# Optimization experiments

Measured on AMD Instinct MI355X. Metric: run time of the kernel, lower is better.

Reference implementation:

```python
import jax, jax.numpy as jnp
import numpy as np

B, L, D = 8, 512, 32      # batch, seq_len, hidden_size (input dim)
N = 64                     # features_nodes (attention neurons)
H = 64                     # interm_layer_size (LSTM hidden)


def setup_inputs() -> dict:
    key = jax.random.key(0)
    ks = jax.random.split(key, 12)
    s = lambda k, shape, fan: jax.random.normal(k, shape, jnp.float32) * (1.0 / np.sqrt(fan))
    return {
        "text": jax.random.normal(ks[0], (B, L, D), jnp.float32),
        # AttentionLSTM params
        "Wx_w": s(ks[1], (N, D), D),
        "Wx_b": jnp.zeros((N,), jnp.float32),
        "Wxhat_w": s(ks[2], (N, D), D),
        "Wxhat_b": jnp.zeros((N,), jnp.float32),
        "att_w": s(ks[3], (1, N), N),
        "att_b": jnp.zeros((1,), jnp.float32),
        # unidirectional LSTM params (PyTorch layout: gates i,f,g,o)
        "W_ih": s(ks[4], (4 * H, D), D),
        "W_hh": s(ks[5], (4 * H, H), H),
        "b_ih": jnp.zeros((4 * H,), jnp.float32),
        "b_hh": jnp.zeros((4 * H,), jnp.float32),
        # dense head
        "dense_w": s(ks[6], (2, H), H),
        "dense_b": jnp.zeros((2,), jnp.float32),
    }


def _forward(text, Wx_w, Wx_b, Wxhat_w, Wxhat_b, att_w, att_b,
             W_ih, W_hh, b_ih, b_hh, dense_w, dense_b):
    # --- AttentionLSTM ---
    Wx = text @ Wx_w.T + Wx_b          # [B,L,N]
    # Wthat[b,i,j,:] = text[b,j,:], so Linear(Wthat) == Wxhat broadcast over i
    Wxhat = text @ Wxhat_w.T + Wxhat_b  # [B,L,N]
    # tanh(Wxhat[b,j] + Wx[b,i]) -> [B,L,L,N]
    t = jnp.tanh(Wxhat[:, None, :, :] + Wx[:, :, None, :])
    A = jax.nn.sigmoid(jnp.einsum('bijn,n->bij', t, att_w[0]) + att_b[0])  # [B,L,L]
    Xatt = jnp.einsum('bij,bjd->bid', A, text)  # sum_j Wthat*A -> [B,L,D]

    # --- unidirectional LSTM (last hidden state only) ---
    h0 = jnp.zeros((text.shape[0], H), text.dtype)
    c0 = jnp.zeros((text.shape[0], H), text.dtype)

    def step(carry, x_t):
        h, c = carry
        gates = x_t @ W_ih.T + b_ih + h @ W_hh.T + b_hh  # [B,4H]
        i, f, g, o = jnp.split(gates, 4, axis=-1)
        c = jax.nn.sigmoid(f) * c + jax.nn.sigmoid(i) * jnp.tanh(g)
        h = jax.nn.sigmoid(o) * jnp.tanh(c)
        return (h, c), None

    (h_last, _), _ = jax.lax.scan(step, (h0, c0), jnp.swapaxes(Xatt, 0, 1))
    return h_last @ dense_w.T + dense_b  # [B,2]


def reference(text, Wx_w, Wx_b, Wxhat_w, Wxhat_b, att_w, att_b,
              W_ih, W_hh, b_ih, b_hh, dense_w, dense_b):
    return _forward(text, Wx_w, Wx_b, Wxhat_w, Wxhat_b, att_w, att_b,
                    W_ih, W_hh, b_ih, b_hh, dense_w, dense_b)
```

## Files before the change

### kernel.cpp

```cpp
#include <hip/hip_runtime.h>
#include <hip/hip_bf16.h>

#define Bb 8
#define Ll 512
#define Dd 32
#define Nn 64
#define Hh 64
#define G4 256

#define L2E  1.4426950408889634f
#define L2E2 2.8853900817779268f

typedef _Float16 h2_t __attribute__((ext_vector_type(2)));

__device__ __forceinline__ float fast_rcp(float x) { return __builtin_amdgcn_rcpf(x); }
__device__ __forceinline__ float fast_exp2(float x) { return __builtin_amdgcn_exp2f(x); }

__device__ __forceinline__ float sig2(float x) {
    return fast_rcp(1.f + fast_exp2(-L2E * x));
}
__device__ __forceinline__ float tanh2(float x) {
    return fmaf(2.f, fast_rcp(1.f + fast_exp2(-L2E2 * x)), -1.f);
}

__device__ __forceinline__ float fdot2(h2_t a, h2_t b, float c) {
#if __has_builtin(__builtin_amdgcn_fdot2)
    return __builtin_amdgcn_fdot2(a, b, c, false);
#else
    return c + (float)a[0] * (float)b[0] + (float)a[1] * (float)b[1];
#endif
}

template<int CTRL>
__device__ __forceinline__ float quad_dpp(float v) {
    return __int_as_float(__builtin_amdgcn_mov_dpp(__float_as_int(v), CTRL, 0xf, 0xf, true));
}
__device__ __forceinline__ float quad_sum(float v) {
    v += quad_dpp<0xB1>(v);
    v += quad_dpp<0x4E>(v);
    return v;
}

__global__ __launch_bounds__(256) void k_proj(
    const float* __restrict__ text,
    const float* __restrict__ Wx_w, const float* __restrict__ Wx_b,
    const float* __restrict__ Wxh_w, const float* __restrict__ Wxh_b,
    float* __restrict__ Ex, float* __restrict__ Eh) {
    int idx = blockIdx.x * 256 + threadIdx.x;
    int n = idx & 63;
    int bl = idx >> 6;
    const float4* tr = (const float4*)(text + bl * Dd);
    const float4* w1 = (const float4*)(Wx_w + n * Dd);
    const float4* w2 = (const float4*)(Wxh_w + n * Dd);
    float a0 = 0.f, a1 = 0.f;
#pragma unroll
    for (int q = 0; q < 8; ++q) {
        float4 t4 = tr[q]; float4 x4 = w1[q]; float4 y4 = w2[q];
        a0 += t4.x * x4.x + t4.y * x4.y + t4.z * x4.z + t4.w * x4.w;
        a1 += t4.x * y4.x + t4.y * y4.y + t4.z * y4.z + t4.w * y4.w;
    }
    Ex[idx] = fast_exp2(L2E2 * (a0 + Wx_b[n]));
    Eh[idx] = fast_exp2(L2E2 * (a1 + Wxh_b[n]));
}

__global__ __launch_bounds__(256) void k_attn(
    const float* __restrict__ text,
    const float* __restrict__ Ex, const float* __restrict__ Eh,
    const float* __restrict__ att_w, const float* __restrict__ att_b,
    const float* __restrict__ W_ih, const float* __restrict__ b_ih,
    const float* __restrict__ b_hh, float* __restrict__ Gx) {
    __shared__ float s_eh[64 * 65];
    __shared__ float s_text[32 * 65];
    __shared__ float2 s_fa[4 * 64];
    __shared__ float s_A[4 * 64];
    __shared__ __align__(16) float s_xatt[4][32];

    int tid = threadIdx.x;
    int bx = blockIdx.x;
    int b = bx >> 7;
    int i0 = (bx & 127) << 2;
    int w = tid >> 6, l = tid & 63;
    int i = i0 + w;

    s_fa[w * 64 + l] = make_float2(Ex[((b * Ll) + i) * Nn + l], att_w[l]);
    float ab = att_b[0];
    __syncthreads();

    float awsum = 0.f;
#pragma unroll
    for (int n = 0; n < 64; ++n) awsum += s_fa[w * 64 + n].y;
    float zc = awsum + ab;

    float xacc = 0.f;
    int d = l & 31, hf = l >> 5;

    for (int jt = 0; jt < 8; ++jt) {
        __syncthreads();
        {
            int n = tid & 63; int j4 = tid >> 6;
#pragma unroll
            for (int r = 0; r < 16; ++r) {
                int jl = j4 + r * 4;
                s_eh[n * 65 + jl] = Eh[((b * Ll) + jt * 64 + jl) * Nn + n];
            }
            int dd = tid & 31; int j8 = tid >> 5;
#pragma unroll
            for (int r = 0; r < 8; ++r) {
                int jl = j8 + r * 8;
                s_text[dd * 65 + jl] = text[((b * Ll) + jt * 64 + jl) * Dd + dd];
            }
        }
        __syncthreads();
        float S = 0.f;
#pragma unroll
        for (int n = 0; n < 64; ++n) {
            float E = s_eh[n * 65 + l];
            float2 fa = s_fa[w * 64 + n];
            float r = fast_rcp(fmaf(E, fa.x, 1.f));
            S = fmaf(fa.y, r, S);
        }
        float A = fast_rcp(1.f + fast_exp2(-L2E * (zc - 2.f * S)));
        s_A[w * 64 + l] = A;
#pragma unroll
        for (int jj = 0; jj < 32; ++jj) {
            int j = hf * 32 + jj;
            xacc += s_A[w * 64 + j] * s_text[d * 65 + j];
        }
    }
    xacc += __shfl_xor(xacc, 32);
    if (l < 32) s_xatt[w][l] = xacc;
    __syncthreads();

    {
        int g = tid;
        const float4* wr = (const float4*)(W_ih + g * Dd);
        float4 wv[8];
#pragma unroll
        for (int q = 0; q < 8; ++q) wv[q] = wr[q];
        float bias = b_ih[g] + b_hh[g];
#pragma unroll
        for (int r = 0; r < 4; ++r) {
            const float4* xr = (const float4*)s_xatt[r];
            float acc = bias;
#pragma unroll
            for (int q = 0; q < 8; ++q) {
                float4 x4 = xr[q]; float4 w4 = wv[q];
                acc += x4.x * w4.x + x4.y * w4.y + x4.z * w4.z + x4.w * w4.w;
            }
            Gx[((b * Ll) + i0 + r) * G4 + g] = acc;
        }
    }
}

__global__ __launch_bounds__(256) void k_lstm(
    const float* __restrict__ Gx, const float* __restrict__ W_hh,
    const float* __restrict__ dense_w, const float* __restrict__ dense_b,
    float* __restrict__ out) {
    __shared__ __align__(16) _Float16 s_h[2][64];
    int b = blockIdx.x;
    int tid = threadIdx.x;
    int w = tid >> 6, l = tid & 63;
    int p = l & 3;
    int u = w * 16 + (l >> 2);

    float pm = (p == 2) ? -L2E2 : -L2E;
    float mo = (p == 2) ? 2.f : 1.f;
    float ao = (p == 2) ? -1.f : 0.f;

    h2_t wreg[4][8];
#pragma unroll
    for (int g = 0; g < 4; ++g) {
        const float4* wp = (const float4*)(W_hh + (g * 64 + u) * 64 + p * 16);
#pragma unroll
        for (int q = 0; q < 4; ++q) {
            float4 v = wp[q];
            wreg[g][2 * q]     = h2_t{(_Float16)v.x, (_Float16)v.y};
            wreg[g][2 * q + 1] = h2_t{(_Float16)v.z, (_Float16)v.w};
        }
    }

    if (tid < 64) s_h[0][tid] = (_Float16)0.f;
    float c = 0.f;
    const float* gxb = Gx + b * Ll * G4;
    int gidx = p * 64 + u;
    float gx_cur = gxb[gidx];
    float gx_n1  = gxb[G4 + gidx];
    __syncthreads();

    int buf = 0;
    for (int t = 0; t < Ll; ++t) {
        int t2 = (t + 2 < Ll) ? (t + 2) : (Ll - 1);
        float gx_n2 = gxb[t2 * G4 + gidx];

        union { float4 f; h2_t h[4]; } u0, u1;
        u0.f = *(const float4*)(&s_h[buf][p * 16]);
        u1.f = *(const float4*)(&s_h[buf][p * 16 + 8]);

        float a0 = (p == 0) ? gx_cur : 0.f;
        float a1 = (p == 1) ? gx_cur : 0.f;
        float a2 = (p == 2) ? gx_cur : 0.f;
        float a3 = (p == 3) ? gx_cur : 0.f;
#pragma unroll
        for (int q = 0; q < 4; ++q) {
            a0 = fdot2(u0.h[q], wreg[0][q], a0);
            a1 = fdot2(u0.h[q], wreg[1][q], a1);
            a2 = fdot2(u0.h[q], wreg[2][q], a2);
            a3 = fdot2(u0.h[q], wreg[3][q], a3);
        }
#pragma unroll
        for (int q = 0; q < 4; ++q) {
            a0 = fdot2(u1.h[q], wreg[0][q + 4], a0);
            a1 = fdot2(u1.h[q], wreg[1][q + 4], a1);
            a2 = fdot2(u1.h[q], wreg[2][q + 4], a2);
            a3 = fdot2(u1.h[q], wreg[3][q + 4], a3);
        }
        float ti = quad_sum(a0);
        float tf = quad_sum(a1);
        float tg = quad_sum(a2);
        float to = quad_sum(a3);
        float tot = (p & 2) ? ((p & 1) ? to : tg) : ((p & 1) ? tf : ti);
        float val = fmaf(mo, fast_rcp(1.f + fast_exp2(pm * tot)), ao);
        float vi = quad_dpp<0x00>(val);
        float vf = quad_dpp<0x55>(val);
        float vg = quad_dpp<0xAA>(val);
        float vo = quad_dpp<0xFF>(val);

        c = fmaf(vf, c, vi * vg);
        float hh = vo * tanh2(c);
        if (p == 0) s_h[buf ^ 1][u] = (_Float16)hh;
        __syncthreads();
        buf ^= 1;
        gx_cur = gx_n1;
        gx_n1 = gx_n2;
    }
    if (tid == 0) {
        float a0 = dense_b[0], a1 = dense_b[1];
        for (int uu = 0; uu < 64; ++uu) {
            float hv = (float)s_h[buf][uu];
            a0 += hv * dense_w[uu];
            a1 += hv * dense_w[64 + uu];
        }
        out[b * 2 + 0] = a0;
        out[b * 2 + 1] = a1;
    }
}

extern "C" void kernel_launch(void* const* d_in, const int* in_sizes, int n_in,
                              void* d_out, int out_size, void* d_ws, size_t ws_size,
                              hipStream_t stream) {
    const float* text    = (const float*)d_in[0];
    const float* Wx_w    = (const float*)d_in[1];
    const float* Wx_b    = (const float*)d_in[2];
    const float* Wxh_w   = (const float*)d_in[3];
    const float* Wxh_b   = (const float*)d_in[4];
    const float* att_w   = (const float*)d_in[5];
    const float* att_b   = (const float*)d_in[6];
    const float* W_ih    = (const float*)d_in[7];
    const float* W_hh    = (const float*)d_in[8];
    const float* b_ih    = (const float*)d_in[9];
    const float* b_hh    = (const float*)d_in[10];
    const float* dense_w = (const float*)d_in[11];
    const float* dense_b = (const float*)d_in[12];

    float* ws   = (float*)d_ws;
    float* Ex   = ws;
    float* Eh   = ws + 262144;
    float* Gx   = ws + 655360;
    float* out  = (float*)d_out;

    hipLaunchKernelGGL(k_proj, dim3((Bb * Ll * Nn) / 256), dim3(256), 0, stream,
                       text, Wx_w, Wx_b, Wxh_w, Wxh_b, Ex, Eh);
    hipLaunchKernelGGL(k_attn, dim3(Bb * (Ll / 4)), dim3(256), 0, stream,
                       text, Ex, Eh, att_w, att_b, W_ih, b_ih, b_hh, Gx);
    hipLaunchKernelGGL(k_lstm, dim3(Bb), dim3(256), 0, stream,
                       Gx, W_hh, dense_w, dense_b, out);
}
```

Before: 203.2 us.

## Run LSTM recurrence in a single wavefront with per-thread full gate rows

Rewrites the LSTM kernel so one 64-thread wavefront handles each batch element. Each thread holds the full W_hh rows for its hidden unit's four gates and computes all gates locally. The attention kernel now writes Gx interleaved by unit so each thread loads one float4 per step. This removes the per-step block barriers and cross-lane DPP reductions, at the cost of 4x serial dot-product work per thread and heavy register use.

```diff
diff --git a/kernel.cpp b/kernel.cpp
--- a/kernel.cpp
+++ b/kernel.cpp
@@ -29,16 +29,6 @@
 #else
     return c + (float)a[0] * (float)b[0] + (float)a[1] * (float)b[1];
 #endif
-}
-
-template<int CTRL>
-__device__ __forceinline__ float quad_dpp(float v) {
-    return __int_as_float(__builtin_amdgcn_mov_dpp(__float_as_int(v), CTRL, 0xf, 0xf, true));
-}
-__device__ __forceinline__ float quad_sum(float v) {
-    v += quad_dpp<0xB1>(v);
-    v += quad_dpp<0x4E>(v);
-    return v;
 }
 
 __global__ __launch_bounds__(256) void k_proj(
@@ -132,12 +122,13 @@
     __syncthreads();
 
     {
-        int g = tid;
-        const float4* wr = (const float4*)(W_ih + g * Dd);
+        int r0 = tid;
+        int gt = r0 >> 6, un = r0 & 63;
+        const float4* wr = (const float4*)(W_ih + r0 * Dd);
         float4 wv[8];
 #pragma unroll
         for (int q = 0; q < 8; ++q) wv[q] = wr[q];
-        float bias = b_ih[g] + b_hh[g];
+        float bias = b_ih[r0] + b_hh[r0];
 #pragma unroll
         for (int r = 0; r < 4; ++r) {
             const float4* xr = (const float4*)s_xatt[r];
@@ -147,101 +138,83 @@
                 float4 x4 = xr[q]; float4 w4 = wv[q];
                 acc += x4.x * w4.x + x4.y * w4.y + x4.z * w4.z + x4.w * w4.w;
             }
-            Gx[((b * Ll) + i0 + r) * G4 + g] = acc;
-        }
-    }
-}
-
-__global__ __launch_bounds__(256) void k_lstm(
+            Gx[((b * Ll) + i0 + r) * G4 + un * 4 + gt] = acc;
+        }
+    }
+}
+
+__global__ __launch_bounds__(64) void k_lstm(
     const float* __restrict__ Gx, const float* __restrict__ W_hh,
     const float* __restrict__ dense_w, const float* __restrict__ dense_b,
     float* __restrict__ out) {
-    __shared__ __align__(16) _Float16 s_h[2][64];
+    __shared__ __align__(16) _Float16 s_h[64];
     int b = blockIdx.x;
-    int tid = threadIdx.x;
-    int w = tid >> 6, l = tid & 63;
-    int p = l & 3;
-    int u = w * 16 + (l >> 2);
-
-    float pm = (p == 2) ? -L2E2 : -L2E;
-    float mo = (p == 2) ? 2.f : 1.f;
-    float ao = (p == 2) ? -1.f : 0.f;
-
-    h2_t wreg[4][8];
+    int l = threadIdx.x;
+
+    h2_t wreg[4][32];
 #pragma unroll
     for (int g = 0; g < 4; ++g) {
-        const float4* wp = (const float4*)(W_hh + (g * 64 + u) * 64 + p * 16);
-#pragma unroll
-        for (int q = 0; q < 4; ++q) {
+        const float4* wp = (const float4*)(W_hh + (g * 64 + l) * 64);
+#pragma unroll
+        for (int q = 0; q < 16; ++q) {
             float4 v = wp[q];
             wreg[g][2 * q]     = h2_t{(_Float16)v.x, (_Float16)v.y};
             wreg[g][2 * q + 1] = h2_t{(_Float16)v.z, (_Float16)v.w};
         }
     }
 
-    if (tid < 64) s_h[0][tid] = (_Float16)0.f;
+    s_h[l] = (_Float16)0.f;
     float c = 0.f;
-    const float* gxb = Gx + b * Ll * G4;
-    int gidx = p * 64 + u;
-    float gx_cur = gxb[gidx];
-    float gx_n1  = gxb[G4 + gidx];
-    __syncthreads();
-
-    int buf = 0;
+    const float4* gxb = (const float4*)Gx + (size_t)b * Ll * 64 + l;
+    float4 gx_cur = gxb[0];
+    float4 gx_n1  = gxb[64];
+
     for (int t = 0; t < Ll; ++t) {
         int t2 = (t + 2 < Ll) ? (t + 2) : (Ll - 1);
-        float gx_n2 = gxb[t2 * G4 + gidx];
-
-        union { float4 f; h2_t h[4]; } u0, u1;
-        u0.f = *(const float4*)(&s_h[buf][p * 16]);
-        u1.f = *(const float4*)(&s_h[buf][p * 16 + 8]);
-
-        float a0 = (p == 0) ? gx_cur : 0.f;
-        float a1 = (p == 1) ? gx_cur : 0.f;
-        float a2 = (p == 2) ? gx_cur : 0.f;
-        float a3 = (p == 3) ? gx_cur : 0.f;
-#pragma unroll
-        for (int q = 0; q < 4; ++q) {
-            a0 = fdot2(u0.h[q], wreg[0][q], a0);
-            a1 = fdot2(u0.h[q], wreg[1][q], a1);
-            a2 = fdot2(u0.h[q], wreg[2][q], a2);
-            a3 = fdot2(u0.h[q], wreg[3][q], a3);
-        }
-#pragma unroll
-        for (int q = 0; q < 4; ++q) {
-            a0 = fdot2(u1.h[q], wreg[0][q + 4], a0);
-            a1 = fdot2(u1.h[q], wreg[1][q + 4], a1);
-            a2 = fdot2(u1.h[q], wreg[2][q + 4], a2);
-            a3 = fdot2(u1.h[q], wreg[3][q + 4], a3);
-        }
-        float ti = quad_sum(a0);
-        float tf = quad_sum(a1);
-        float tg = quad_sum(a2);
-        float to = quad_sum(a3);
-        float tot = (p & 2) ? ((p & 1) ? to : tg) : ((p & 1) ? tf : ti);
-        float val = fmaf(mo, fast_rcp(1.f + fast_exp2(pm * tot)), ao);
-        float vi = quad_dpp<0x00>(val);
-        float vf = quad_dpp<0x55>(val);
-        float vg = quad_dpp<0xAA>(val);
-        float vo = quad_dpp<0xFF>(val);
-
-        c = fmaf(vf, c, vi * vg);
-        float hh = vo * tanh2(c);
-        if (p == 0) s_h[buf ^ 1][u] = (_Float16)hh;
-        __syncthreads();
-        buf ^= 1;
+        float4 gx_n2 = gxb[(size_t)t2 * 64];
+
+        h2_t hreg[32];
+        const float4* hb = (const float4*)s_h;
+#pragma unroll
+        for (int q = 0; q < 8; ++q) {
+            union { float4 f; h2_t h[4]; } uu;
+            uu.f = hb[q];
+            hreg[4 * q]     = uu.h[0];
+            hreg[4 * q + 1] = uu.h[1];
+            hreg[4 * q + 2] = uu.h[2];
+            hreg[4 * q + 3] = uu.h[3];
+        }
+
+        float a0 = gx_cur.x, a1 = gx_cur.y, a2 = gx_cur.z, a3 = gx_cur.w;
+        float b0 = 0.f, b1 = 0.f, b2 = 0.f, b3 = 0.f;
+#pragma unroll
+        for (int k = 0; k < 16; ++k) {
+            a0 = fdot2(hreg[k], wreg[0][k], a0);
+            a1 = fdot2(hreg[k], wreg[1][k], a1);
+            a2 = fdot2(hreg[k], wreg[2][k], a2);
+            a3 = fdot2(hreg[k], wreg[3][k], a3);
+            b0 = fdot2(hreg[k + 16], wreg[0][k + 16], b0);
+            b1 = fdot2(hreg[k + 16], wreg[1][k + 16], b1);
+            b2 = fdot2(hreg[k + 16], wreg[2][k + 16], b2);
+            b3 = fdot2(hreg[k + 16], wreg[3][k + 16], b3);
+        }
+        float ti = a0 + b0, tf = a1 + b1, tg = a2 + b2, to = a3 + b3;
+
+        float gi = sig2(ti);
+        float gf = sig2(tf);
+        float gg = tanh2(tg);
+        float go = sig2(to);
+        c = fmaf(gf, c, gi * gg);
+        float hh = go * tanh2(c);
+        s_h[l] = (_Float16)hh;
         gx_cur = gx_n1;
         gx_n1 = gx_n2;
     }
-    if (tid == 0) {
-        float a0 = dense_b[0], a1 = dense_b[1];
-        for (int uu = 0; uu < 64; ++uu) {
-            float hv = (float)s_h[buf][uu];
-            a0 += hv * dense_w[uu];
-            a1 += hv * dense_w[64 + uu];
-        }
-        out[b * 2 + 0] = a0;
-        out[b * 2 + 1] = a1;
+    if (l < 2) {
+        float a = dense_b[l];
+        for (int uu = 0; uu < 64; ++uu)
+            a += (float)s_h[uu] * dense_w[l * 64 + uu];
+        out[b * 2 + l] = a;
     }
 }
 
@@ -272,6 +245,6 @@
                        text, Wx_w, Wx_b, Wxh_w, Wxh_b, Ex, Eh);
     hipLaunchKernelGGL(k_attn, dim3(Bb * (Ll / 4)), dim3(256), 0, stream,
                        text, Ex, Eh, att_w, att_b, W_ih, b_ih, b_hh, Gx);
-    hipLaunchKernelGGL(k_lstm, dim3(Bb), dim3(256), 0, stream,
+    hipLaunchKernelGGL(k_lstm, dim3(Bb), dim3(64), 0, stream,
                        Gx, W_hh, dense_w, dense_b, out);
 }
```

After: 279.3 us. +37.5%, slower.

## Transpose Eh tile layout for vectorized LDS reads; compute all LSTM gates per lane

Applied to the files above, without the earlier changes.

The attention kernel now stores the Eh tile row-major per j with a padded stride of 66, so each lane reads its row with float2 loads alongside float4 reads of the att factors. The A·text reduction is vectorized to float2 loads. In the LSTM, each lane computes all four gate activations redundantly instead of one activation per lane followed by four DPP broadcasts. This shortens the serial per-step dependency chain at the cost of more transcendental operations per lane. The row-major layout with stride 66 may cause LDS bank conflicts, since lanes stride 66 floats apart.

```diff
diff --git a/kernel.cpp b/kernel.cpp
--- a/kernel.cpp
+++ b/kernel.cpp
@@ -69,8 +69,8 @@
     const float* __restrict__ att_w, const float* __restrict__ att_b,
     const float* __restrict__ W_ih, const float* __restrict__ b_ih,
     const float* __restrict__ b_hh, float* __restrict__ Gx) {
-    __shared__ float s_eh[64 * 65];
-    __shared__ float s_text[32 * 65];
+    __shared__ float s_eh[64 * 66];
+    __shared__ float s_text[32 * 66];
     __shared__ float2 s_fa[4 * 64];
     __shared__ float s_A[4 * 64];
     __shared__ __align__(16) float s_xatt[4][32];
@@ -101,30 +101,36 @@
 #pragma unroll
             for (int r = 0; r < 16; ++r) {
                 int jl = j4 + r * 4;
-                s_eh[n * 65 + jl] = Eh[((b * Ll) + jt * 64 + jl) * Nn + n];
+                s_eh[jl * 66 + n] = Eh[((b * Ll) + jt * 64 + jl) * Nn + n];
             }
             int dd = tid & 31; int j8 = tid >> 5;
 #pragma unroll
             for (int r = 0; r < 8; ++r) {
                 int jl = j8 + r * 8;
-                s_text[dd * 65 + jl] = text[((b * Ll) + jt * 64 + jl) * Dd + dd];
+                s_text[dd * 66 + jl] = text[((b * Ll) + jt * 64 + jl) * Dd + dd];
             }
         }
         __syncthreads();
         float S = 0.f;
-#pragma unroll
-        for (int n = 0; n < 64; ++n) {
-            float E = s_eh[n * 65 + l];
-            float2 fa = s_fa[w * 64 + n];
-            float r = fast_rcp(fmaf(E, fa.x, 1.f));
-            S = fmaf(fa.y, r, S);
+        const float* ehrow = &s_eh[l * 66];
+        const float2* farow = &s_fa[w * 64];
+#pragma unroll
+        for (int n = 0; n < 64; n += 2) {
+            float2 E2 = *(const float2*)(ehrow + n);
+            float4 fa2 = *(const float4*)(farow + n);
+            float r0 = fast_rcp(fmaf(E2.x, fa2.x, 1.f));
+            S = fmaf(fa2.y, r0, S);
+            float r1 = fast_rcp(fmaf(E2.y, fa2.z, 1.f));
+            S = fmaf(fa2.w, r1, S);
         }
         float A = fast_rcp(1.f + fast_exp2(-L2E * (zc - 2.f * S)));
         s_A[w * 64 + l] = A;
 #pragma unroll
-        for (int jj = 0; jj < 32; ++jj) {
+        for (int jj = 0; jj < 32; jj += 2) {
             int j = hf * 32 + jj;
-            xacc += s_A[w * 64 + j] * s_text[d * 65 + j];
+            float2 A2 = *(const float2*)&s_A[w * 64 + j];
+            float2 T2 = *(const float2*)&s_text[d * 66 + j];
+            xacc = fmaf(A2.x, T2.x, fmaf(A2.y, T2.y, xacc));
         }
     }
     xacc += __shfl_xor(xacc, 32);
@@ -132,12 +138,12 @@
     __syncthreads();
 
     {
-        int g = tid;
-        const float4* wr = (const float4*)(W_ih + g * Dd);
+        int r0 = tid;
+        const float4* wr = (const float4*)(W_ih + r0 * Dd);
         float4 wv[8];
 #pragma unroll
         for (int q = 0; q < 8; ++q) wv[q] = wr[q];
-        float bias = b_ih[g] + b_hh[g];
+        float bias = b_ih[r0] + b_hh[r0];
 #pragma unroll
         for (int r = 0; r < 4; ++r) {
             const float4* xr = (const float4*)s_xatt[r];
@@ -147,7 +153,7 @@
                 float4 x4 = xr[q]; float4 w4 = wv[q];
                 acc += x4.x * w4.x + x4.y * w4.y + x4.z * w4.z + x4.w * w4.w;
             }
-            Gx[((b * Ll) + i0 + r) * G4 + g] = acc;
+            Gx[((b * Ll) + i0 + r) * G4 + r0] = acc;
         }
     }
 }
@@ -163,10 +169,6 @@
     int p = l & 3;
     int u = w * 16 + (l >> 2);
 
-    float pm = (p == 2) ? -L2E2 : -L2E;
-    float mo = (p == 2) ? 2.f : 1.f;
-    float ao = (p == 2) ? -1.f : 0.f;
-
     h2_t wreg[4][8];
 #pragma unroll
     for (int g = 0; g < 4; ++g) {
@@ -181,7 +183,7 @@
 
     if (tid < 64) s_h[0][tid] = (_Float16)0.f;
     float c = 0.f;
-    const float* gxb = Gx + b * Ll * G4;
+    const float* gxb = Gx + (size_t)b * Ll * G4;
     int gidx = p * 64 + u;
     float gx_cur = gxb[gidx];
     float gx_n1  = gxb[G4 + gidx];
@@ -190,7 +192,7 @@
     int buf = 0;
     for (int t = 0; t < Ll; ++t) {
         int t2 = (t + 2 < Ll) ? (t + 2) : (Ll - 1);
-        float gx_n2 = gxb[t2 * G4 + gidx];
+        float gx_n2 = gxb[(size_t)t2 * G4 + gidx];
 
         union { float4 f; h2_t h[4]; } u0, u1;
         u0.f = *(const float4*)(&s_h[buf][p * 16]);
@@ -218,15 +220,13 @@
         float tf = quad_sum(a1);
         float tg = quad_sum(a2);
         float to = quad_sum(a3);
-        float tot = (p & 2) ? ((p & 1) ? to : tg) : ((p & 1) ? tf : ti);
-        float val = fmaf(mo, fast_rcp(1.f + fast_exp2(pm * tot)), ao);
-        float vi = quad_dpp<0x00>(val);
-        float vf = quad_dpp<0x55>(val);
-        float vg = quad_dpp<0xAA>(val);
-        float vo = quad_dpp<0xFF>(val);
-
-        c = fmaf(vf, c, vi * vg);
-        float hh = vo * tanh2(c);
+
+        float gi = sig2(ti);
+        float gf = sig2(tf);
+        float gg = tanh2(tg);
+        float go = sig2(to);
+        c = fmaf(gf, c, gi * gg);
+        float hh = go * tanh2(c);
         if (p == 0) s_h[buf ^ 1][u] = (_Float16)hh;
         __syncthreads();
         buf ^= 1;
```

Result: no change. 200.1 us (-1.5%).
